# Optimization experiments

Hardware: AMD Instinct MI355X
Metric: run time of the kernel (lower is better)

Reference implementation:

```python
import jax, jax.numpy as jnp
import numpy as np
from jax import lax

B, T = 128, 512
V, D = 100000, 100   # word vocab, word embedding dim
H = 100              # per-direction LSTM hidden (concat -> 200)
L = 25               # number of CRF labels


def setup_inputs() -> dict:
    key = jax.random.key(0)
    ks = jax.random.split(key, 16)
    s = 0.02
    inp = {
        "tok_tensor": jax.random.randint(ks[0], (B, T), 0, V, dtype=jnp.int32),
        "tag_tensor": jax.random.randint(ks[1], (B, T), 0, L, dtype=jnp.int32),
        "lengths": jnp.full((B,), T, dtype=jnp.int32),
        "word_emb": jax.random.normal(ks[2], (V, D), jnp.float32) * s,
        # forward-direction LSTM (PyTorch gate order i,f,g,o)
        "w_ih_f": jax.random.normal(ks[3], (4 * H, D), jnp.float32) * s,
        "w_hh_f": jax.random.normal(ks[4], (4 * H, H), jnp.float32) * s,
        "b_ih_f": jax.random.normal(ks[5], (4 * H,), jnp.float32) * s,
        "b_hh_f": jax.random.normal(ks[6], (4 * H,), jnp.float32) * s,
        # backward-direction LSTM
        "w_ih_b": jax.random.normal(ks[7], (4 * H, D), jnp.float32) * s,
        "w_hh_b": jax.random.normal(ks[8], (4 * H, H), jnp.float32) * s,
        "b_ih_b": jax.random.normal(ks[9], (4 * H,), jnp.float32) * s,
        "b_hh_b": jax.random.normal(ks[10], (4 * H,), jnp.float32) * s,
        # hidden2tag linear
        "w_tag": jax.random.normal(ks[11], (L, 2 * H), jnp.float32) * s,
        "b_tag": jax.random.normal(ks[12], (L,), jnp.float32) * s,
        # CRF params
        "transitions": jax.random.normal(ks[13], (L, L), jnp.float32) * 0.1,
        "start_trans": jax.random.normal(ks[14], (L,), jnp.float32) * 0.1,
        "end_trans": jax.random.normal(ks[15], (L,), jnp.float32) * 0.1,
    }
    return inp


def _lstm(x_tbd, w_ih, w_hh, b_ih, b_hh, reverse):
    """x_tbd: [T,B,D] -> hidden states [T,B,H], aligned with input time axis."""
    Bh = x_tbd.shape[1]
    Hh = w_hh.shape[1]
    h0 = jnp.zeros((Bh, Hh), x_tbd.dtype)
    c0 = jnp.zeros((Bh, Hh), x_tbd.dtype)

    def step(carry, xt):
        h, c = carry
        gates = xt @ w_ih.T + b_ih + h @ w_hh.T + b_hh
        i, f, g, o = jnp.split(gates, 4, axis=-1)
        i = jax.nn.sigmoid(i); f = jax.nn.sigmoid(f)
        g = jnp.tanh(g); o = jax.nn.sigmoid(o)
        c = f * c + i * g
        h = o * jnp.tanh(c)
        return (h, c), h

    _, hs = lax.scan(step, (h0, c0), x_tbd, reverse=reverse)
    return hs


def _crf_nll(emissions, tags, mask, transitions, start_trans, end_trans):
    """Sum over batch of -(gold path score - log partition).
    emissions: [B,T,L], tags: [B,T] int, mask: [B,T] float (1=valid)."""
    Bb = emissions.shape[0]
    b_idx = jnp.arange(Bb)
    em_t = emissions.transpose(1, 0, 2)   # [T,B,L]
    tags_t = tags.T                       # [T,B]
    mask_t = mask.T                       # [T,B]

    # --- gold path score ---
    first_tags = tags_t[0]
    score0 = start_trans[first_tags] + em_t[0][b_idx, first_tags]

    def num_step(score, inp):
        em, tp, tc, m = inp  # emissions[t], tags[t-1], tags[t], mask[t]
        s = transitions[tp, tc] + em[b_idx, tc]
        return score + m * s, None

    gold, _ = lax.scan(num_step, score0,
                       (em_t[1:], tags_t[:-1], tags_t[1:], mask_t[1:]))
    last_idx = jnp.sum(mask, axis=1).astype(jnp.int32) - 1
    last_tags = tags[b_idx, last_idx]
    gold = gold + end_trans[last_tags]

    # --- log partition (forward algorithm) ---
    alpha0 = start_trans + em_t[0]  # [B,L]

    def part_step(alpha, inp):
        em, m = inp
        # [B,L_prev,1] + [L_prev,L_next] + [B,1,L_next]
        nxt = jax.nn.logsumexp(alpha[:, :, None] + transitions[None] + em[:, None, :], axis=1)
        alpha = jnp.where(m[:, None] > 0, nxt, alpha)
        return alpha, None

    alpha, _ = lax.scan(part_step, alpha0, (em_t[1:], mask_t[1:]))
    logZ = jax.nn.logsumexp(alpha + end_trans, axis=1)
    return jnp.sum(logZ - gold)


def reference(tok_tensor, tag_tensor, lengths,
              word_emb, w_ih_f, w_hh_f, b_ih_f, b_hh_f,
              w_ih_b, w_hh_b, b_ih_b, b_hh_b,
              w_tag, b_tag, transitions, start_trans, end_trans):
    # word embedding lookup: [B,T,D]
    tok_embs = word_emb[tok_tensor]
    x_tbd = tok_embs.transpose(1, 0, 2)  # [T,B,D]
    # BiLSTM encoder (dropout off: eval / deterministic reference)
    h_fwd = _lstm(x_tbd, w_ih_f, w_hh_f, b_ih_f, b_hh_f, reverse=False)
    h_bwd = _lstm(x_tbd, w_ih_b, w_hh_b, b_ih_b, b_hh_b, reverse=True)
    seq = jnp.concatenate([h_fwd, h_bwd], axis=-1).transpose(1, 0, 2)  # [B,T,2H]
    # hidden2tag
    emissions = jnp.einsum('btd,ld->btl', seq, w_tag) + b_tag  # [B,T,L]
    # CRF negative log-likelihood
    mask = (jnp.arange(T)[None, :] < lengths[:, None]).astype(emissions.dtype)
    return _crf_nll(emissions, tag_tensor, mask, transitions, start_trans, end_trans)
```

## Files before the change

### kernel.cpp

```cpp
#include <hip/hip_runtime.h>
#include <cstdint>
#include <cstddef>

#define BB 128
#define TT 512
#define DD 100
#define HH 100
#define NG 400
#define LL 25
#define TS 32
#define NTILE 16
#define F_LOG2E 1.44269504088896340736f
#define F_LN2   0.69314718055994530942f

typedef __decltype(__builtin_amdgcn_cvt_pkrtz(0.f, 0.f)) h2_t;
typedef _Float16 v8h __attribute__((ext_vector_type(8)));
typedef float v4f __attribute__((ext_vector_type(4)));

__device__ __forceinline__ h2_t bc_h2(unsigned int u) {
  return __builtin_bit_cast(h2_t, u);
}
__device__ __forceinline__ unsigned int pk(float x, float y) {
  return __builtin_bit_cast(unsigned int, __builtin_amdgcn_cvt_pkrtz(x, y));
}

__device__ __forceinline__ float fdot2(h2_t a, h2_t b, float c) {
#if __has_builtin(__builtin_amdgcn_fdot2)
  return __builtin_amdgcn_fdot2(a, b, c, false);
#else
  return c + (float)a[0] * (float)b[0] + (float)a[1] * (float)b[1];
#endif
}

__device__ __forceinline__ float fexp2(float x) { return __builtin_amdgcn_exp2f(x); }
__device__ __forceinline__ float flog2(float x) { return __builtin_amdgcn_logf(x); }
__device__ __forceinline__ float frcp(float x)  { return __builtin_amdgcn_rcpf(x); }

__device__ __forceinline__ float sigmoid_f(float x) {
  return frcp(1.f + fexp2(-F_LOG2E * x));
}
__device__ __forceinline__ float tanh_f(float x) {
  float e = fexp2(2.f * F_LOG2E * x);
  return 1.f - 2.f * frcp(e + 1.f);
}

template <int CTRL>
__device__ __forceinline__ float qadd(float v) {
#if __has_builtin(__builtin_amdgcn_mov_dpp)
  int m = __builtin_amdgcn_mov_dpp(__builtin_bit_cast(int, v), CTRL, 0xF, 0xF, true);
  return v + __builtin_bit_cast(float, m);
#else
  int x = (CTRL == 177) ? 1 : 2;
  return v + __shfl_xor(v, x);
#endif
}

template <int LANE>
__device__ __forceinline__ float qbcast(float v) {
#if __has_builtin(__builtin_amdgcn_mov_dpp)
  int m = __builtin_amdgcn_mov_dpp(__builtin_bit_cast(int, v), LANE * 0x55, 0xF, 0xF, true);
  return __builtin_bit_cast(float, m);
#else
  return __shfl(v, (threadIdx.x & 63 & ~3) + LANE);
#endif
}

__device__ __forceinline__ float bperm(float v, int byteidx) {
  return __builtin_bit_cast(float,
      __builtin_amdgcn_ds_bpermute(byteidx, __builtin_bit_cast(int, v)));
}
__device__ __forceinline__ float rfl(float v) {
  return __builtin_bit_cast(float,
      __builtin_amdgcn_readfirstlane(__builtin_bit_cast(int, v)));
}

__device__ __forceinline__ void lds_barrier() {
  __builtin_amdgcn_s_waitcnt(0xC07F);
  __builtin_amdgcn_s_barrier();
}

__global__ __launch_bounds__(512, 2) void lstm_fused2(
    const int* __restrict__ tok, const float* __restrict__ emb,
    const float* __restrict__ w_ih_f, const float* __restrict__ w_ih_b,
    const float* __restrict__ b_ih_f, const float* __restrict__ b_hh_f,
    const float* __restrict__ b_ih_b, const float* __restrict__ b_hh_b,
    const float* __restrict__ w_hh_f, const float* __restrict__ w_hh_b,
    const float* __restrict__ w_tag, const float* __restrict__ b_tag,
    float* __restrict__ em_f, float* __restrict__ em_b)
{
  const int tid = threadIdx.x;
  const int b   = blockIdx.x & 127;
  const int dir = blockIdx.x >> 7;
  const float* w_hh = dir ? w_hh_b : w_hh_f;
  const float* w_ih = dir ? w_ih_b : w_ih_f;
  const float* b_ih = dir ? b_ih_b : b_ih_f;
  const float* b_hh = dir ? b_hh_b : b_hh_f;

  __shared__ __align__(16) unsigned int wlds[400 * 68];
  __shared__ __align__(16) unsigned short gin_lds[TS * 400];
  __shared__ __align__(16) unsigned int xlds[TS * 68];
  __shared__ __align__(16) unsigned int hls0[52];
  __shared__ __align__(16) unsigned int hls1[52];

  for (int i = tid; i < 400 * 25; i += 512) {
    int row = i / 25;
    int q = i - row * 25;
    const float4 v = *(const float4*)(w_ih + (size_t)row * DD + 4 * q);
    wlds[row * 68 + 2 * q]     = pk(v.x, v.y);
    wlds[row * 68 + 2 * q + 1] = pk(v.z, v.w);
  }
  for (int i = tid; i < 400 * 18; i += 512) {
    int row = i / 18;
    int d = i - row * 18;
    wlds[row * 68 + 50 + d] = 0u;
  }
  for (int i = tid; i < TS * 18; i += 512) {
    int row = i / 18;
    int d = i - row * 18;
    xlds[row * 68 + 50 + d] = 0u;
  }

  const bool uact = tid < NG;
  const int j = tid >> 2;
  const int s = tid & 3;
  const int od = 12 * s;
  const int nnv = (s == 3) ? 14 : 12;

  h2_t wA[14], wB[14], wC[14], wD[14];
  float bias = 0.f;
  if (uact) {
#pragma unroll
    for (int d = 0; d < 14; ++d) {
      int dd = (d < nnv) ? (od + d) : 0;
      const float* r0 = w_hh + (size_t)(0 * 100 + j) * HH + 2 * dd;
      const float* r1 = w_hh + (size_t)(1 * 100 + j) * HH + 2 * dd;
      const float* r2 = w_hh + (size_t)(2 * 100 + j) * HH + 2 * dd;
      const float* r3 = w_hh + (size_t)(3 * 100 + j) * HH + 2 * dd;
      h2_t z = __builtin_amdgcn_cvt_pkrtz(0.f, 0.f);
      wA[d] = (d < nnv) ? __builtin_amdgcn_cvt_pkrtz(r0[0], r0[1]) : z;
      wB[d] = (d < nnv) ? __builtin_amdgcn_cvt_pkrtz(r1[0], r1[1]) : z;
      wC[d] = (d < nnv) ? __builtin_amdgcn_cvt_pkrtz(r2[0], r2[1]) : z;
      wD[d] = (d < nnv) ? __builtin_amdgcn_cvt_pkrtz(r3[0], r3[1]) : z;
    }
    bias = b_ih[s * 100 + j] + b_hh[s * 100 + j];
  }
  const float kk2 = (s == 2) ? (2.f * F_LOG2E) : (-F_LOG2E);
  const float cA  = (s == 2) ? -2.f : 1.f;
  const float cB  = (s == 2) ? 1.f : 0.f;

  const int el = tid - 448;
  const bool eact = (el >= 0) && (el < 50);
  const int l  = (el >= 0) ? (el >> 1) : 0;
  const int hf = (el >= 0) ? (el & 1) : 0;
  const int eo = hf ? 24 : 0;
  const int en = hf ? 26 : 24;
  h2_t wt[26];
  float bt = 0.f;
  if (eact) {
    const float* wr = w_tag + (size_t)l * 200 + dir * 100;
#pragma unroll
    for (int d = 0; d < 26; ++d) {
      int dd = (d < en) ? (eo + d) : 0;
      h2_t z = __builtin_amdgcn_cvt_pkrtz(0.f, 0.f);
      wt[d] = (d < en) ? __builtin_amdgcn_cvt_pkrtz(wr[2 * dd], wr[2 * dd + 1]) : z;
    }
    if (dir == 0 && hf == 0) bt = b_tag[l];
  }
  float* emo = dir ? em_b : em_f;
  float* emp = emo + ((size_t)b * TT + (dir ? (TT - 1) : 0)) * LL + l;
  const ptrdiff_t estep = dir ? -(ptrdiff_t)LL : (ptrdiff_t)LL;

  if (tid < 52) { hls0[tid] = 0u; hls1[tid] = 0u; }

  const int wv   = tid >> 6;
  const int lane = tid & 63;
  const int l16  = lane & 15;
  const int quad = lane >> 4;
  const int c0b  = (25 * wv) >> 3;
  const int c1b  = (25 * (wv + 1)) >> 3;

  const int tprow = tid / 13;
  const int tps   = tid - 13 * tprow;
  const bool tp_act = tid < 416;

  float4 xa = {0, 0, 0, 0}, xb = {0, 0, 0, 0};
  if (tp_act) {
    int ii = tprow;
    int tt = dir ? (TT - 1 - ii) : ii;
    int tk = tok[b * TT + tt];
    const float* xp = emb + (size_t)tk * DD + 8 * tps;
    xa = *(const float4*)xp;
    if (tps < 12) xb = *(const float4*)(xp + 4);
  }

  float c = 0.f;
  unsigned short gnext = 0;
  int grow = 0;

#define SDOT(d, hh) \
  p0 = fdot2(wA[d], bc_h2(hh), p0); p1 = fdot2(wB[d], bc_h2(hh), p1); \
  p2 = fdot2(wC[d], bc_h2(hh), p2); p3 = fdot2(wD[d], bc_h2(hh), p3);
#define EDOT(d, hh) { h2_t h = bc_h2(hh); \
  if ((d & 3) == 0) a0 = fdot2(wt[d], h, a0); \
  else if ((d & 3) == 1) a1 = fdot2(wt[d], h, a1); \
  else if ((d & 3) == 2) a2 = fdot2(wt[d], h, a2); \
  else a3 = fdot2(wt[d], h, a3); }

#define SCAN_STEP(HRD, HWR, TVNZ)                                          \
  {                                                                        \
    if (uact) {                                                            \
      unsigned short gcurr = gnext;                                        \
      int nr = (grow < TS - 1) ? grow + 1 : TS - 1;                        \
      gnext = gin_lds[nr * 400 + tid];                                     \
      grow = nr;                                                           \
      const unsigned int* hp = (HRD) + od;                                 \
      uint4 u0 = *((const uint4*)hp);                                      \
      uint4 u1 = *((const uint4*)(hp + 4));                                \
      uint4 u2 = *((const uint4*)(hp + 8));                                \
      uint2 u3 = *((const uint2*)(hp + 12));                               \
      float p0, p1, p2, p3;                                                \
      p0 = fdot2(wA[0], bc_h2(u0.x), 0.f);                                 \
      p1 = fdot2(wB[0], bc_h2(u0.x), 0.f);                                 \
      p2 = fdot2(wC[0], bc_h2(u0.x), 0.f);                                 \
      p3 = fdot2(wD[0], bc_h2(u0.x), 0.f);                                 \
      SDOT(1, u0.y)  SDOT(2, u0.z)  SDOT(3, u0.w)                          \
      SDOT(4, u1.x)  SDOT(5, u1.y)  SDOT(6, u1.z)  SDOT(7, u1.w)           \
      SDOT(8, u2.x)  SDOT(9, u2.y)  SDOT(10, u2.z) SDOT(11, u2.w)          \
      SDOT(12, u3.x) SDOT(13, u3.y)                                        \
      p0 = qadd<78>(qadd<177>(p0));                                        \
      p1 = qadd<78>(qadd<177>(p1));                                        \
      p2 = qadd<78>(qadd<177>(p2));                                        \
      p3 = qadd<78>(qadd<177>(p3));                                        \
      float psel = (s == 0) ? p0 : (s == 1) ? p1 : (s == 2) ? p2 : p3;     \
      float gate = psel + bias + (float)__builtin_bit_cast(__fp16, gcurr); \
      float y  = fexp2(kk2 * gate);                                        \
      float rr = frcp(1.f + y);                                            \
      float actv = fmaf(cA, rr, cB);                                       \
      float iv = qbcast<0>(actv);                                          \
      float fv = qbcast<1>(actv);                                          \
      float gv = qbcast<2>(actv);                                          \
      float ov = qbcast<3>(actv);                                          \
      c = fmaf(fv, c, iv * gv);                                            \
      float hvv = ov * tanh_f(c);                                          \
      if (s == 0) ((__fp16*)(HWR))[j] = (__fp16)hvv;                       \
    } else if (eact && (TVNZ)) {                                           \
      const unsigned int* hp = (HRD) + eo;                                 \
      uint4 e0 = *((const uint4*)hp);                                      \
      uint4 e1 = *((const uint4*)(hp + 4));                                \
      uint4 e2 = *((const uint4*)(hp + 8));                                \
      uint4 e3 = *((const uint4*)(hp + 12));                               \
      uint4 e4 = *((const uint4*)(hp + 16));                               \
      uint4 e5 = *((const uint4*)(hp + 20));                               \
      uint2 e6 = *((const uint2*)(hp + 24));                               \
      float a0, a1, a2, a3;                                                \
      a0 = fdot2(wt[0], bc_h2(e0.x), 0.f);                                 \
      a1 = fdot2(wt[1], bc_h2(e0.y), 0.f);                                 \
      a2 = fdot2(wt[2], bc_h2(e0.z), 0.f);                                 \
      a3 = fdot2(wt[3], bc_h2(e0.w), 0.f);                                 \
      EDOT(4, e1.x)  EDOT(5, e1.y)  EDOT(6, e1.z)  EDOT(7, e1.w)           \
      EDOT(8, e2.x)  EDOT(9, e2.y)  EDOT(10, e2.z) EDOT(11, e2.w)          \
      EDOT(12, e3.x) EDOT(13, e3.y) EDOT(14, e3.z) EDOT(15, e3.w)          \
      EDOT(16, e4.x) EDOT(17, e4.y) EDOT(18, e4.z) EDOT(19, e4.w)          \
      EDOT(20, e5.x) EDOT(21, e5.y) EDOT(22, e5.z) EDOT(23, e5.w)          \
      EDOT(24, e6.x) EDOT(25, e6.y)                                        \
      float ss = (a0 + a1) + (a2 + a3);                                    \
      float tot = qadd<177>(ss);                                           \
      if (hf == 0) *emp = tot + bt;                                        \
      emp += estep;                                                        \
    }                                                                      \
    lds_barrier();                                                         \
  }

  __syncthreads();

  for (int T = 0; T < NTILE; ++T) {
    if (tp_act) {
      unsigned int* xr = xlds + tprow * 68 + 4 * tps;
      if (tps < 12) {
        uint4 u;
        u.x = pk(xa.x, xa.y); u.y = pk(xa.z, xa.w);
        u.z = pk(xb.x, xb.y); u.w = pk(xb.z, xb.w);
        *(uint4*)xr = u;
      } else {
        xr[0] = pk(xa.x, xa.y);
        xr[1] = pk(xa.z, xa.w);
      }
    }
    __syncthreads();

    {
      v8h af[2][4];
#pragma unroll
      for (int rg = 0; rg < 2; ++rg)
#pragma unroll
        for (int f = 0; f < 4; ++f)
          af[rg][f] = __builtin_bit_cast(v8h,
              *(const uint4*)(xlds + (rg * 16 + l16) * 68 + f * 16 + quad * 4));

      if (tp_act && T + 1 < NTILE) {
        int ii = (T + 1) * TS + tprow;
        int tt = dir ? (TT - 1 - ii) : ii;
        int tk = tok[b * TT + tt];
        const float* xp = emb + (size_t)tk * DD + 8 * tps;
        xa = *(const float4*)xp;
        if (tps < 12) xb = *(const float4*)(xp + 4);
      }

      __fp16* gout = (__fp16*)gin_lds;
      for (int cc = c0b; cc < c1b; ++cc) {
        const int n = 16 * cc + l16;
        const unsigned int* wp = wlds + n * 68 + quad * 4;
        v8h bf0 = __builtin_bit_cast(v8h, *(const uint4*)(wp));
        v8h bf1 = __builtin_bit_cast(v8h, *(const uint4*)(wp + 16));
        v8h bf2 = __builtin_bit_cast(v8h, *(const uint4*)(wp + 32));
        v8h bf3 = __builtin_bit_cast(v8h, *(const uint4*)(wp + 48));
        const int qn = (n * 41) >> 12;
        const int p  = ((n - 100 * qn) << 2) + qn;
#pragma unroll
        for (int rg = 0; rg < 2; ++rg) {
          v4f acc = {0.f, 0.f, 0.f, 0.f};
          acc = __builtin_amdgcn_mfma_f32_16x16x32_f16(af[rg][0], bf0, acc, 0, 0, 0);
          acc = __builtin_amdgcn_mfma_f32_16x16x32_f16(af[rg][1], bf1, acc, 0, 0, 0);
          acc = __builtin_amdgcn_mfma_f32_16x16x32_f16(af[rg][2], bf2, acc, 0, 0, 0);
          acc = __builtin_amdgcn_mfma_f32_16x16x32_f16(af[rg][3], bf3, acc, 0, 0, 0);
          const int rowb = rg * 16 + quad * 4;
#pragma unroll
          for (int r = 0; r < 4; ++r)
            gout[(rowb + r) * 400 + p] = (__fp16)acc[r];
        }
      }
    }
    __syncthreads();
    if (uact) { grow = 0; gnext = gin_lds[tid]; }

    SCAN_STEP(hls0, hls1, (T > 0))
    SCAN_STEP(hls1, hls0, true)
    for (int it = 1; it < TS / 2; ++it) {
      SCAN_STEP(hls0, hls1, true)
      SCAN_STEP(hls1, hls0, true)
    }
  }
#undef SCAN_STEP
#undef SDOT

  if (eact) {
    const unsigned int* hp = hls0 + eo;
    uint4 e0 = *((const uint4*)hp);
    uint4 e1 = *((const uint4*)(hp + 4));
    uint4 e2 = *((const uint4*)(hp + 8));
    uint4 e3 = *((const uint4*)(hp + 12));
    uint4 e4 = *((const uint4*)(hp + 16));
    uint4 e5 = *((const uint4*)(hp + 20));
    uint2 e6 = *((const uint2*)(hp + 24));
    float a0, a1, a2, a3;
    a0 = fdot2(wt[0], bc_h2(e0.x), 0.f);
    a1 = fdot2(wt[1], bc_h2(e0.y), 0.f);
    a2 = fdot2(wt[2], bc_h2(e0.z), 0.f);
    a3 = fdot2(wt[3], bc_h2(e0.w), 0.f);
    EDOT(4, e1.x)  EDOT(5, e1.y)  EDOT(6, e1.z)  EDOT(7, e1.w)
    EDOT(8, e2.x)  EDOT(9, e2.y)  EDOT(10, e2.z) EDOT(11, e2.w)
    EDOT(12, e3.x) EDOT(13, e3.y) EDOT(14, e3.z) EDOT(15, e3.w)
    EDOT(16, e4.x) EDOT(17, e4.y) EDOT(18, e4.z) EDOT(19, e4.w)
    EDOT(20, e5.x) EDOT(21, e5.y) EDOT(22, e5.z) EDOT(23, e5.w)
    EDOT(24, e6.x) EDOT(25, e6.y)
    float ss = (a0 + a1) + (a2 + a3);
    float tot = qadd<177>(ss);
    if (hf == 0) {
      int ttp = dir ? 0 : (TT - 1);
      emo[((size_t)b * TT + ttp) * LL + l] = tot + bt;
    }
  }
#undef EDOT
}

__global__ __launch_bounds__(512, 2) void lstm_scan_fb(
    const int* __restrict__ tok, const float* __restrict__ emb,
    const float* __restrict__ w_ih_f, const float* __restrict__ w_hh_f,
    const float* __restrict__ b_ih_f, const float* __restrict__ b_hh_f,
    const float* __restrict__ w_ih_b, const float* __restrict__ w_hh_b,
    const float* __restrict__ b_ih_b, const float* __restrict__ b_hh_b,
    unsigned short* __restrict__ hc16)
{
  const int tid = threadIdx.x;
  const int b   = blockIdx.x & 127;
  const int dir = blockIdx.x >> 7;

  const float* w_ih = dir ? w_ih_b : w_ih_f;
  const float* w_hh = dir ? w_hh_b : w_hh_f;
  const float* b_ih = dir ? b_ih_b : b_ih_f;
  const float* b_hh = dir ? b_hh_b : b_hh_f;

  __shared__ __align__(16) unsigned int xs[2][64];
  __shared__ __align__(16) unsigned int hls[64];
  __shared__ float gl[NG];

  h2_t wih[50], whh[50];
  float bias = 0.f;
  if (tid < NG) {
    const float4* wi = (const float4*)(w_ih + tid * DD);
    const float4* wh = (const float4*)(w_hh + tid * DD);
#pragma unroll
    for (int kk = 0; kk < 25; ++kk) {
      float4 a = wi[kk];
      wih[2 * kk]     = __builtin_amdgcn_cvt_pkrtz(a.x, a.y);
      wih[2 * kk + 1] = __builtin_amdgcn_cvt_pkrtz(a.z, a.w);
      float4 c = wh[kk];
      whh[2 * kk]     = __builtin_amdgcn_cvt_pkrtz(c.x, c.y);
      whh[2 * kk + 1] = __builtin_amdgcn_cvt_pkrtz(c.z, c.w);
    }
    bias = b_ih[tid] + b_hh[tid];
  }
  if (tid < 2) { xs[0][50 + tid] = 0u; xs[1][50 + tid] = 0u; hls[50 + tid] = 0u; }
  if (tid < 50) hls[tid] = 0u;

  const int base = b * TT;
  if (tid >= 448 && tid < 498) {
    int tt0 = dir ? (TT - 1) : 0;
    int i = tid - 448;
    int tk = tok[base + tt0];
    float2 v = ((const float2*)(emb + (size_t)tk * DD))[i];
    xs[0][i] = pk(v.x, v.y);
  }
  __syncthreads();

  float cst = 0.f;
  unsigned short* hcb = hc16 + (size_t)base * 200 + dir * 100;

  for (int t = 0; t < TT; ++t) {
    const int buf = t & 1;
    const int tt  = dir ? (TT - 1 - t) : t;

    if (tid < NG) {
      float a0 = bias, a1 = 0.f, a2 = 0.f, a3 = 0.f;
      const unsigned int* xp = xs[buf];
#pragma unroll
      for (int g = 0; g < 13; ++g) {
        uint4 u = ((const uint4*)xp)[g];
        const int k = 4 * g;
        a0 = fdot2(wih[k], bc_h2(u.x), a0);
        a1 = fdot2(wih[k + 1], bc_h2(u.y), a1);
        if (k + 2 < 50) a2 = fdot2(wih[k + 2], bc_h2(u.z), a2);
        if (k + 3 < 50) a3 = fdot2(wih[k + 3], bc_h2(u.w), a3);
      }
#pragma unroll
      for (int g = 0; g < 13; ++g) {
        uint4 u = ((const uint4*)hls)[g];
        const int k = 4 * g;
        a0 = fdot2(whh[k], bc_h2(u.x), a0);
        a1 = fdot2(whh[k + 1], bc_h2(u.y), a1);
        if (k + 2 < 50) a2 = fdot2(whh[k + 2], bc_h2(u.z), a2);
        if (k + 3 < 50) a3 = fdot2(whh[k + 3], bc_h2(u.w), a3);
      }
      float accs = (a0 + a1) + (a2 + a3);
      float av = (tid >= 200 && tid < 300) ? tanh_f(accs) : sigmoid_f(accs);
      gl[tid] = av;
    } else if (tid >= 448 && tid < 498 && t < TT - 1) {
      int ttn = dir ? (TT - 2 - t) : (t + 1);
      int i = tid - 448;
      int tk = tok[base + ttn];
      float2 v = ((const float2*)(emb + (size_t)tk * DD))[i];
      xs[buf ^ 1][i] = pk(v.x, v.y);
    }
    __syncthreads();

    if (tid < HH) {
      float gi = gl[tid], gf = gl[tid + 100], gg = gl[tid + 200], go = gl[tid + 300];
      cst = gf * cst + gi * gg;
      float hv = go * tanh_f(cst);
      __fp16 h16 = (__fp16)hv;
      ((__fp16*)hls)[tid] = h16;
      hcb[(size_t)tt * 200 + tid] = __builtin_bit_cast(unsigned short, h16);
    }
    __syncthreads();
  }
}

__global__ __launch_bounds__(256, 2) void emis2(
    const unsigned short* __restrict__ hc16, const float* __restrict__ w_tag,
    const float* __restrict__ b_tag, float* __restrict__ em)
{
  __shared__ unsigned int hsh[64 * 101];
  __shared__ unsigned int wsh[25 * 100];
  const int tid = threadIdx.x;
  const size_t m0 = (size_t)blockIdx.x * 64;

  const unsigned int* hcu = (const unsigned int*)hc16;
  for (int i = tid; i < 64 * 100; i += 256) {
    int r = i / 100;
    int k = i - r * 100;
    hsh[r * 101 + k] = hcu[m0 * 100 + i];
  }
  for (int i = tid; i < 25 * 100; i += 256) {
    float2 wv = ((const float2*)w_tag)[i];
    wsh[i] = pk(wv.x, wv.y);
  }
  __syncthreads();

  const int r = tid & 63, q = tid >> 6;
  int lidx[7];
  bool lv[7];
  float acc[7];
#pragma unroll
  for (int ii = 0; ii < 7; ++ii) {
    int l = q + 4 * ii;
    lv[ii] = (l < LL);
    lidx[ii] = lv[ii] ? l : 0;
    acc[ii] = lv[ii] ? b_tag[lidx[ii]] : 0.f;
  }
  const unsigned int* hrow = hsh + r * 101;
#pragma unroll 2
  for (int k = 0; k < 100; ++k) {
    h2_t hv = bc_h2(hrow[k]);
#pragma unroll
    for (int ii = 0; ii < 7; ++ii)
      acc[ii] = fdot2(hv, bc_h2(wsh[lidx[ii] * 100 + k]), acc[ii]);
  }
#pragma unroll
  for (int ii = 0; ii < 7; ++ii)
    if (lv[ii]) em[(m0 + r) * LL + lidx[ii]] = acc[ii];
}

__global__ __launch_bounds__(192) void crf_all(
    const float* __restrict__ em_f, const float* __restrict__ em_b,
    const int* __restrict__ tags, const int* __restrict__ lengths,
    const float* __restrict__ trans,
    const float* __restrict__ startt, const float* __restrict__ endt,
    float* __restrict__ out)
{
  const int tid = threadIdx.x;
  const int b   = blockIdx.x;
  const int w   = tid >> 6;
  const int lane = tid & 63;

  __shared__ float abf[LL], abb[LL];
  __shared__ float gd;

  if (w < 2) {
    const int side = w;
    const int j = (lane < LL) ? lane : 0;
    const float* ef = em_f + (size_t)b * TT * LL;
    const float* eb = em_b + (size_t)b * TT * LL;

    float E[LL];
#pragma unroll
    for (int i = 0; i < LL; ++i) {
      float tv = (side == 0 ? trans[i * LL + j] : trans[j * LL + i]);
      E[i] = fexp2(tv * F_LOG2E);
    }

    float a, C = 0.f;
    if (side == 0) {
      a = (startt[j] + ef[j] + eb[j]) * F_LOG2E;
      float efA = ef[LL + j],     ebA = eb[LL + j];
      float efB = ef[2 * LL + j], ebB = eb[2 * LL + j];
      for (int t = 1; t < 256; ++t) {
        float em2 = (efA + ebA) * F_LOG2E;
        int tn = (t + 2 < 256) ? (t + 2) : 255;
        efA = efB; ebA = ebB;
        efB = ef[(size_t)tn * LL + j];
        ebB = eb[(size_t)tn * LL + j];
        float sh = rfl(a);
        C += sh;
        float A = fexp2(a - sh);
        float s0 = 0.f, s1 = 0.f, s2 = 0.f, s3 = 0.f;
#pragma unroll
        for (int i = 0; i < LL; ++i) {
          float Ai = bperm(A, 4 * i);
          if ((i & 3) == 0) s0 = fmaf(Ai, E[i], s0);
          else if ((i & 3) == 1) s1 = fmaf(Ai, E[i], s1);
          else if ((i & 3) == 2) s2 = fmaf(Ai, E[i], s2);
          else s3 = fmaf(Ai, E[i], s3);
        }
        a = flog2((s0 + s1) + (s2 + s3)) + em2;
      }
    } else {
      a = endt[j] * F_LOG2E;
      float efA = ef[(size_t)(TT - 1) * LL + j], ebA = eb[(size_t)(TT - 1) * LL + j];
      float efB = ef[(size_t)(TT - 2) * LL + j], ebB = eb[(size_t)(TT - 2) * LL + j];
      for (int stpi = 0; stpi < 256; ++stpi) {
        float em2 = (efA + ebA) * F_LOG2E;
        int t1n = (stpi + 2 < 256) ? (TT - 3 - stpi) : 256;
        efA = efB; ebA = ebB;
        efB = ef[(size_t)t1n * LL + j];
        ebB = eb[(size_t)t1n * LL + j];
        float v = a + em2;
        float sh = rfl(v);
        C += sh;
        float A = fexp2(v - sh);
        float s0 = 0.f, s1 = 0.f, s2 = 0.f, s3 = 0.f;
#pragma unroll
        for (int i = 0; i < LL; ++i) {
          float Ai = bperm(A, 4 * i);
          if ((i & 3) == 0) s0 = fmaf(Ai, E[i], s0);
          else if ((i & 3) == 1) s1 = fmaf(Ai, E[i], s1);
          else if ((i & 3) == 2) s2 = fmaf(Ai, E[i], s2);
          else s3 = fmaf(Ai, E[i], s3);
        }
        a = flog2((s0 + s1) + (s2 + s3));
      }
    }
    if (lane < LL) {
      if (side == 0) abf[lane] = a + C;
      else          abb[lane] = a + C;
    }
  } else {
    const int len = lengths[b];
    float acc = 0.f;
#pragma unroll
    for (int k = 0; k < 8; ++k) {
      int t = k * 64 + lane;
      int tg = tags[b * TT + t];
      size_t ei = ((size_t)b * TT + t) * LL + tg;
      float e = em_f[ei] + em_b[ei];
      float term;
      if (t == 0) term = startt[tg] + e;
      else        term = trans[tags[b * TT + t - 1] * LL + tg] + e;
      if (t == len - 1) term += endt[tg];
      if (t < len) acc += term;
    }
    for (int o = 32; o > 0; o >>= 1) acc += __shfl_down(acc, o);
    if (lane == 0) gd = acc;
  }
  __syncthreads();

  if (tid < 64) {
    float v = (tid < LL) ? (abf[tid] + abb[tid]) : -1e30f;
    float m = v;
    for (int o = 32; o > 0; o >>= 1) m = fmaxf(m, __shfl_down(m, o));
    m = rfl(m);
    float e = (tid < LL) ? fexp2(v - m) : 0.f;
    for (int o = 32; o > 0; o >>= 1) e += __shfl_down(e, o);
    if (tid == 0)
      atomicAdd(out, (m + flog2(e)) * F_LN2 - gd);
  }
}

extern "C" void kernel_launch(void* const* d_in, const int* in_sizes, int n_in,
                              void* d_out, int out_size, void* d_ws, size_t ws_size,
                              hipStream_t stream) {
  const int*   tok   = (const int*)d_in[0];
  const int*   tags  = (const int*)d_in[1];
  const int*   lens  = (const int*)d_in[2];
  const float* emb   = (const float*)d_in[3];
  const float* wif   = (const float*)d_in[4];
  const float* whf   = (const float*)d_in[5];
  const float* bif   = (const float*)d_in[6];
  const float* bhf   = (const float*)d_in[7];
  const float* wib   = (const float*)d_in[8];
  const float* whb   = (const float*)d_in[9];
  const float* bib   = (const float*)d_in[10];
  const float* bhb   = (const float*)d_in[11];
  const float* wtag  = (const float*)d_in[12];
  const float* btag  = (const float*)d_in[13];
  const float* trans = (const float*)d_in[14];
  const float* st    = (const float*)d_in[15];
  const float* en    = (const float*)d_in[16];

  char* wsb = (char*)d_ws;
  float* em_f = (float*)wsb;
  float* em_b = (float*)(wsb + 6553600);
  const size_t need_fused = 13107200ULL;
  const size_t need_fb    = 13107200ULL + 26214400ULL;

  hipMemsetAsync(d_out, 0, sizeof(float), stream);

  if (ws_size >= need_fused && ws_size < need_fb) {
    lstm_fused2<<<256, 512, 0, stream>>>(tok, emb, wif, wib, bif, bhf, bib, bhb,
                                         whf, whb, wtag, btag, em_f, em_b);
  } else if (ws_size >= need_fb) {
    lstm_fused2<<<256, 512, 0, stream>>>(tok, emb, wif, wib, bif, bhf, bib, bhb,
                                         whf, whb, wtag, btag, em_f, em_b);
  } else {
    unsigned short* hc16 = (unsigned short*)(wsb + 13107200);
    hipMemsetAsync(em_b, 0, 6553600, stream);
    lstm_scan_fb<<<256, 512, 0, stream>>>(tok, emb, wif, whf, bif, bhf,
                                          wib, whb, bib, bhb, hc16);
    emis2<<<1024, 256, 0, stream>>>(hc16, wtag, btag, em_f);
  }
  crf_all<<<128, 192, 0, stream>>>(em_f, em_b, tags, lens, trans, st, en,
                                   (float*)d_out);
}
```

Baseline: 433.1 us.

## Keep input-projection weights in MFMA registers and use LDS broadcast in CRF scan

New measurement: 424.9 us (median of 2 runs). No clear change (-1.9%).

```diff
diff --git a/kernel.cpp b/kernel.cpp
--- a/kernel.cpp
+++ b/kernel.cpp
@@ -65,21 +65,23 @@
 #endif
 }
 
-__device__ __forceinline__ float bperm(float v, int byteidx) {
-  return __builtin_bit_cast(float,
-      __builtin_amdgcn_ds_bpermute(byteidx, __builtin_bit_cast(int, v)));
-}
 __device__ __forceinline__ float rfl(float v) {
   return __builtin_bit_cast(float,
       __builtin_amdgcn_readfirstlane(__builtin_bit_cast(int, v)));
 }
 
+__device__ __forceinline__ void wave_fence() {
+#if __has_builtin(__builtin_amdgcn_wave_barrier)
+  __builtin_amdgcn_wave_barrier();
+#endif
+}
+
 __device__ __forceinline__ void lds_barrier() {
   __builtin_amdgcn_s_waitcnt(0xC07F);
   __builtin_amdgcn_s_barrier();
 }
 
-__global__ __launch_bounds__(512, 2) void lstm_fused2(
+__global__ __launch_bounds__(512, 2) void lstm_fused3(
     const int* __restrict__ tok, const float* __restrict__ emb,
     const float* __restrict__ w_ih_f, const float* __restrict__ w_ih_b,
     const float* __restrict__ b_ih_f, const float* __restrict__ b_hh_f,
@@ -96,24 +98,48 @@
   const float* b_ih = dir ? b_ih_b : b_ih_f;
   const float* b_hh = dir ? b_hh_b : b_hh_f;
 
-  __shared__ __align__(16) unsigned int wlds[400 * 68];
   __shared__ __align__(16) unsigned short gin_lds[TS * 400];
   __shared__ __align__(16) unsigned int xlds[TS * 68];
   __shared__ __align__(16) unsigned int hls0[52];
   __shared__ __align__(16) unsigned int hls1[52];
 
-  for (int i = tid; i < 400 * 25; i += 512) {
-    int row = i / 25;
-    int q = i - row * 25;
-    const float4 v = *(const float4*)(w_ih + (size_t)row * DD + 4 * q);
-    wlds[row * 68 + 2 * q]     = pk(v.x, v.y);
-    wlds[row * 68 + 2 * q + 1] = pk(v.z, v.w);
-  }
-  for (int i = tid; i < 400 * 18; i += 512) {
-    int row = i / 18;
-    int d = i - row * 18;
-    wlds[row * 68 + 50 + d] = 0u;
-  }
+  const int wv   = tid >> 6;
+  const int lane = tid & 63;
+  const int l16  = lane & 15;
+  const int quad = lane >> 4;
+  const int c0b  = (25 * wv) >> 3;
+  const int c1b  = (25 * (wv + 1)) >> 3;
+  const int ncol = c1b - c0b;
+
+  v8h bfr[4][4];
+  int pcol[4];
+#pragma unroll
+  for (int ci = 0; ci < 4; ++ci) {
+    const int cc = (ci < ncol) ? (c0b + ci) : c0b;
+    const int n  = 16 * cc + l16;
+    const float* wr = w_ih + (size_t)n * DD;
+#pragma unroll
+    for (int f = 0; f < 3; ++f) {
+      const float* wp = wr + f * 32 + quad * 8;
+      float4 va = *(const float4*)(wp);
+      float4 vb = *(const float4*)(wp + 4);
+      uint4 u;
+      u.x = pk(va.x, va.y); u.y = pk(va.z, va.w);
+      u.z = pk(vb.x, vb.y); u.w = pk(vb.z, vb.w);
+      bfr[ci][f] = __builtin_bit_cast(v8h, u);
+    }
+    {
+      uint4 u = {0u, 0u, 0u, 0u};
+      if (quad == 0) {
+        float4 va = *(const float4*)(wr + 96);
+        u.x = pk(va.x, va.y); u.y = pk(va.z, va.w);
+      }
+      bfr[ci][3] = __builtin_bit_cast(v8h, u);
+    }
+    const int qn = (n * 41) >> 12;
+    pcol[ci] = ((n - 100 * qn) << 2) + qn;
+  }
+
   for (int i = tid; i < TS * 18; i += 512) {
     int row = i / 18;
     int d = i - row * 18;
@@ -171,13 +197,6 @@
   const ptrdiff_t estep = dir ? -(ptrdiff_t)LL : (ptrdiff_t)LL;
 
   if (tid < 52) { hls0[tid] = 0u; hls1[tid] = 0u; }
-
-  const int wv   = tid >> 6;
-  const int lane = tid & 63;
-  const int l16  = lane & 15;
-  const int quad = lane >> 4;
-  const int c0b  = (25 * wv) >> 3;
-  const int c1b  = (25 * (wv + 1)) >> 3;
 
   const int tprow = tid / 13;
   const int tps   = tid - 13 * tprow;
@@ -307,22 +326,17 @@
       }
 
       __fp16* gout = (__fp16*)gin_lds;
-      for (int cc = c0b; cc < c1b; ++cc) {
-        const int n = 16 * cc + l16;
-        const unsigned int* wp = wlds + n * 68 + quad * 4;
-        v8h bf0 = __builtin_bit_cast(v8h, *(const uint4*)(wp));
-        v8h bf1 = __builtin_bit_cast(v8h, *(const uint4*)(wp + 16));
-        v8h bf2 = __builtin_bit_cast(v8h, *(const uint4*)(wp + 32));
-        v8h bf3 = __builtin_bit_cast(v8h, *(const uint4*)(wp + 48));
-        const int qn = (n * 41) >> 12;
-        const int p  = ((n - 100 * qn) << 2) + qn;
+#pragma unroll
+      for (int ci = 0; ci < 4; ++ci) {
+        if (ci >= ncol) break;
+        const int p = pcol[ci];
 #pragma unroll
         for (int rg = 0; rg < 2; ++rg) {
           v4f acc = {0.f, 0.f, 0.f, 0.f};
-          acc = __builtin_amdgcn_mfma_f32_16x16x32_f16(af[rg][0], bf0, acc, 0, 0, 0);
-          acc = __builtin_amdgcn_mfma_f32_16x16x32_f16(af[rg][1], bf1, acc, 0, 0, 0);
-          acc = __builtin_amdgcn_mfma_f32_16x16x32_f16(af[rg][2], bf2, acc, 0, 0, 0);
-          acc = __builtin_amdgcn_mfma_f32_16x16x32_f16(af[rg][3], bf3, acc, 0, 0, 0);
+          acc = __builtin_amdgcn_mfma_f32_16x16x32_f16(af[rg][0], bfr[ci][0], acc, 0, 0, 0);
+          acc = __builtin_amdgcn_mfma_f32_16x16x32_f16(af[rg][1], bfr[ci][1], acc, 0, 0, 0);
+          acc = __builtin_amdgcn_mfma_f32_16x16x32_f16(af[rg][2], bfr[ci][2], acc, 0, 0, 0);
+          acc = __builtin_amdgcn_mfma_f32_16x16x32_f16(af[rg][3], bfr[ci][3], acc, 0, 0, 0);
           const int rowb = rg * 16 + quad * 4;
 #pragma unroll
           for (int r = 0; r < 4; ++r)
@@ -373,154 +387,7 @@
 #undef EDOT
 }
 
-__global__ __launch_bounds__(512, 2) void lstm_scan_fb(
-    const int* __restrict__ tok, const float* __restrict__ emb,
-    const float* __restrict__ w_ih_f, const float* __restrict__ w_hh_f,
-    const float* __restrict__ b_ih_f, const float* __restrict__ b_hh_f,
-    const float* __restrict__ w_ih_b, const float* __restrict__ w_hh_b,
-    const float* __restrict__ b_ih_b, const float* __restrict__ b_hh_b,
-    unsigned short* __restrict__ hc16)
-{
-  const int tid = threadIdx.x;
-  const int b   = blockIdx.x & 127;
-  const int dir = blockIdx.x >> 7;
-
-  const float* w_ih = dir ? w_ih_b : w_ih_f;
-  const float* w_hh = dir ? w_hh_b : w_hh_f;
-  const float* b_ih = dir ? b_ih_b : b_ih_f;
-  const float* b_hh = dir ? b_hh_b : b_hh_f;
-
-  __shared__ __align__(16) unsigned int xs[2][64];
-  __shared__ __align__(16) unsigned int hls[64];
-  __shared__ float gl[NG];
-
-  h2_t wih[50], whh[50];
-  float bias = 0.f;
-  if (tid < NG) {
-    const float4* wi = (const float4*)(w_ih + tid * DD);
-    const float4* wh = (const float4*)(w_hh + tid * DD);
-#pragma unroll
-    for (int kk = 0; kk < 25; ++kk) {
-      float4 a = wi[kk];
-      wih[2 * kk]     = __builtin_amdgcn_cvt_pkrtz(a.x, a.y);
-      wih[2 * kk + 1] = __builtin_amdgcn_cvt_pkrtz(a.z, a.w);
-      float4 c = wh[kk];
-      whh[2 * kk]     = __builtin_amdgcn_cvt_pkrtz(c.x, c.y);
-      whh[2 * kk + 1] = __builtin_amdgcn_cvt_pkrtz(c.z, c.w);
-    }
-    bias = b_ih[tid] + b_hh[tid];
-  }
-  if (tid < 2) { xs[0][50 + tid] = 0u; xs[1][50 + tid] = 0u; hls[50 + tid] = 0u; }
-  if (tid < 50) hls[tid] = 0u;
-
-  const int base = b * TT;
-  if (tid >= 448 && tid < 498) {
-    int tt0 = dir ? (TT - 1) : 0;
-    int i = tid - 448;
-    int tk = tok[base + tt0];
-    float2 v = ((const float2*)(emb + (size_t)tk * DD))[i];
-    xs[0][i] = pk(v.x, v.y);
-  }
-  __syncthreads();
-
-  float cst = 0.f;
-  unsigned short* hcb = hc16 + (size_t)base * 200 + dir * 100;
-
-  for (int t = 0; t < TT; ++t) {
-    const int buf = t & 1;
-    const int tt  = dir ? (TT - 1 - t) : t;
-
-    if (tid < NG) {
-      float a0 = bias, a1 = 0.f, a2 = 0.f, a3 = 0.f;
-      const unsigned int* xp = xs[buf];
-#pragma unroll
-      for (int g = 0; g < 13; ++g) {
-        uint4 u = ((const uint4*)xp)[g];
-        const int k = 4 * g;
-        a0 = fdot2(wih[k], bc_h2(u.x), a0);
-        a1 = fdot2(wih[k + 1], bc_h2(u.y), a1);
-        if (k + 2 < 50) a2 = fdot2(wih[k + 2], bc_h2(u.z), a2);
-        if (k + 3 < 50) a3 = fdot2(wih[k + 3], bc_h2(u.w), a3);
-      }
-#pragma unroll
-      for (int g = 0; g < 13; ++g) {
-        uint4 u = ((const uint4*)hls)[g];
-        const int k = 4 * g;
-        a0 = fdot2(whh[k], bc_h2(u.x), a0);
-        a1 = fdot2(whh[k + 1], bc_h2(u.y), a1);
-        if (k + 2 < 50) a2 = fdot2(whh[k + 2], bc_h2(u.z), a2);
-        if (k + 3 < 50) a3 = fdot2(whh[k + 3], bc_h2(u.w), a3);
-      }
-      float accs = (a0 + a1) + (a2 + a3);
-      float av = (tid >= 200 && tid < 300) ? tanh_f(accs) : sigmoid_f(accs);
-      gl[tid] = av;
-    } else if (tid >= 448 && tid < 498 && t < TT - 1) {
-      int ttn = dir ? (TT - 2 - t) : (t + 1);
-      int i = tid - 448;
-      int tk = tok[base + ttn];
-      float2 v = ((const float2*)(emb + (size_t)tk * DD))[i];
-      xs[buf ^ 1][i] = pk(v.x, v.y);
-    }
-    __syncthreads();
-
-    if (tid < HH) {
-      float gi = gl[tid], gf = gl[tid + 100], gg = gl[tid + 200], go = gl[tid + 300];
-      cst = gf * cst + gi * gg;
-      float hv = go * tanh_f(cst);
-      __fp16 h16 = (__fp16)hv;
-      ((__fp16*)hls)[tid] = h16;
-      hcb[(size_t)tt * 200 + tid] = __builtin_bit_cast(unsigned short, h16);
-    }
-    __syncthreads();
-  }
-}
-
-__global__ __launch_bounds__(256, 2) void emis2(
-    const unsigned short* __restrict__ hc16, const float* __restrict__ w_tag,
-    const float* __restrict__ b_tag, float* __restrict__ em)
-{
-  __shared__ unsigned int hsh[64 * 101];
-  __shared__ unsigned int wsh[25 * 100];
-  const int tid = threadIdx.x;
-  const size_t m0 = (size_t)blockIdx.x * 64;
-
-  const unsigned int* hcu = (const unsigned int*)hc16;
-  for (int i = tid; i < 64 * 100; i += 256) {
-    int r = i / 100;
-    int k = i - r * 100;
-    hsh[r * 101 + k] = hcu[m0 * 100 + i];
-  }
-  for (int i = tid; i < 25 * 100; i += 256) {
-    float2 wv = ((const float2*)w_tag)[i];
-    wsh[i] = pk(wv.x, wv.y);
-  }
-  __syncthreads();
-
-  const int r = tid & 63, q = tid >> 6;
-  int lidx[7];
-  bool lv[7];
-  float acc[7];
-#pragma unroll
-  for (int ii = 0; ii < 7; ++ii) {
-    int l = q + 4 * ii;
-    lv[ii] = (l < LL);
-    lidx[ii] = lv[ii] ? l : 0;
-    acc[ii] = lv[ii] ? b_tag[lidx[ii]] : 0.f;
-  }
-  const unsigned int* hrow = hsh + r * 101;
-#pragma unroll 2
-  for (int k = 0; k < 100; ++k) {
-    h2_t hv = bc_h2(hrow[k]);
-#pragma unroll
-    for (int ii = 0; ii < 7; ++ii)
-      acc[ii] = fdot2(hv, bc_h2(wsh[lidx[ii] * 100 + k]), acc[ii]);
-  }
-#pragma unroll
-  for (int ii = 0; ii < 7; ++ii)
-    if (lv[ii]) em[(m0 + r) * LL + lidx[ii]] = acc[ii];
-}
-
-__global__ __launch_bounds__(192) void crf_all(
+__global__ __launch_bounds__(192) void crf_all2(
     const float* __restrict__ em_f, const float* __restrict__ em_b,
     const int* __restrict__ tags, const int* __restrict__ lengths,
     const float* __restrict__ trans,
@@ -532,20 +399,53 @@
   const int w   = tid >> 6;
   const int lane = tid & 63;
 
+  __shared__ __align__(16) float As[2][32];
   __shared__ float abf[LL], abb[LL];
   __shared__ float gd;
+
+  if (w < 2 && lane >= LL && lane < 32) As[w][lane] = 0.f;
 
   if (w < 2) {
     const int side = w;
     const int j = (lane < LL) ? lane : 0;
     const float* ef = em_f + (size_t)b * TT * LL;
     const float* eb = em_b + (size_t)b * TT * LL;
-
-    float E[LL];
+    float* Aw = As[side];
+    const float4* Ap = (const float4*)Aw;
+
+    float E[28];
 #pragma unroll
     for (int i = 0; i < LL; ++i) {
       float tv = (side == 0 ? trans[i * LL + j] : trans[j * LL + i]);
       E[i] = fexp2(tv * F_LOG2E);
+    }
+    E[25] = 0.f; E[26] = 0.f; E[27] = 0.f;
+
+#define LSE_STEP(vin, aout)                                                \
+    {                                                                      \
+      float sh = rfl(vin);                                                 \
+      C += sh;                                                             \
+      float A = fexp2((vin) - sh);                                         \
+      if (lane < LL) Aw[lane] = A;                                         \
+      wave_fence();                                                        \
+      float4 q0 = Ap[0], q1 = Ap[1], q2 = Ap[2], q3 = Ap[3];               \
+      float4 q4 = Ap[4], q5 = Ap[5], q6 = Ap[6];                           \
+      float s0, s1, s2, s3;                                                \
+      s0 = q0.x * E[0];  s1 = q0.y * E[1];                                 \
+      s2 = q0.z * E[2];  s3 = q0.w * E[3];                                 \
+      s0 = fmaf(q1.x, E[4], s0);  s1 = fmaf(q1.y, E[5], s1);               \
+      s2 = fmaf(q1.z, E[6], s2);  s3 = fmaf(q1.w, E[7], s3);               \
+      s0 = fmaf(q2.x, E[8], s0);  s1 = fmaf(q2.y, E[9], s1);               \
+      s2 = fmaf(q2.z, E[10], s2); s3 = fmaf(q2.w, E[11], s3);              \
+      s0 = fmaf(q3.x, E[12], s0); s1 = fmaf(q3.y, E[13], s1);              \
+      s2 = fmaf(q3.z, E[14], s2); s3 = fmaf(q3.w, E[15], s3);              \
+      s0 = fmaf(q4.x, E[16], s0); s1 = fmaf(q4.y, E[17], s1);              \
+      s2 = fmaf(q4.z, E[18], s2); s3 = fmaf(q4.w, E[19], s3);              \
+      s0 = fmaf(q5.x, E[20], s0); s1 = fmaf(q5.y, E[21], s1);              \
+      s2 = fmaf(q5.z, E[22], s2); s3 = fmaf(q5.w, E[23], s3);              \
+      s0 = fmaf(q6.x, E[24], s0); s1 = fmaf(q6.y, E[25], s1);              \
+      s2 = fmaf(q6.z, E[26], s2); s3 = fmaf(q6.w, E[27], s3);              \
+      aout = flog2((s0 + s1) + (s2 + s3));                                 \
     }
 
     float a, C = 0.f;
@@ -559,19 +459,9 @@
         efA = efB; ebA = ebB;
         efB = ef[(size_t)tn * LL + j];
         ebB = eb[(size_t)tn * LL + j];
-        float sh = rfl(a);
-        C += sh;
-        float A = fexp2(a - sh);
-        float s0 = 0.f, s1 = 0.f, s2 = 0.f, s3 = 0.f;
-#pragma unroll
-        for (int i = 0; i < LL; ++i) {
-          float Ai = bperm(A, 4 * i);
-          if ((i & 3) == 0) s0 = fmaf(Ai, E[i], s0);
-          else if ((i & 3) == 1) s1 = fmaf(Ai, E[i], s1);
-          else if ((i & 3) == 2) s2 = fmaf(Ai, E[i], s2);
-          else s3 = fmaf(Ai, E[i], s3);
-        }
-        a = flog2((s0 + s1) + (s2 + s3)) + em2;
+        float nx;
+        LSE_STEP(a, nx)
+        a = nx + em2;
       }
     } else {
       a = endt[j] * F_LOG2E;
@@ -584,21 +474,10 @@
         efB = ef[(size_t)t1n * LL + j];
         ebB = eb[(size_t)t1n * LL + j];
         float v = a + em2;
-        float sh = rfl(v);
-        C += sh;
-        float A = fexp2(v - sh);
-        float s0 = 0.f, s1 = 0.f, s2 = 0.f, s3 = 0.f;
-#pragma unroll
-        for (int i = 0; i < LL; ++i) {
-          float Ai = bperm(A, 4 * i);
-          if ((i & 3) == 0) s0 = fmaf(Ai, E[i], s0);
-          else if ((i & 3) == 1) s1 = fmaf(Ai, E[i], s1);
-          else if ((i & 3) == 2) s2 = fmaf(Ai, E[i], s2);
-          else s3 = fmaf(Ai, E[i], s3);
-        }
-        a = flog2((s0 + s1) + (s2 + s3));
+        LSE_STEP(v, a)
       }
     }
+#undef LSE_STEP
     if (lane < LL) {
       if (side == 0) abf[lane] = a + C;
       else          abb[lane] = a + C;
@@ -659,24 +538,11 @@
   char* wsb = (char*)d_ws;
   float* em_f = (float*)wsb;
   float* em_b = (float*)(wsb + 6553600);
-  const size_t need_fused = 13107200ULL;
-  const size_t need_fb    = 13107200ULL + 26214400ULL;
 
   hipMemsetAsync(d_out, 0, sizeof(float), stream);
 
-  if (ws_size >= need_fused && ws_size < need_fb) {
-    lstm_fused2<<<256, 512, 0, stream>>>(tok, emb, wif, wib, bif, bhf, bib, bhb,
-                                         whf, whb, wtag, btag, em_f, em_b);
-  } else if (ws_size >= need_fb) {
-    lstm_fused2<<<256, 512, 0, stream>>>(tok, emb, wif, wib, bif, bhf, bib, bhb,
-                                         whf, whb, wtag, btag, em_f, em_b);
-  } else {
-    unsigned short* hc16 = (unsigned short*)(wsb + 13107200);
-    hipMemsetAsync(em_b, 0, 6553600, stream);
-    lstm_scan_fb<<<256, 512, 0, stream>>>(tok, emb, wif, whf, bif, bhf,
-                                          wib, whb, bib, bhb, hc16);
-    emis2<<<1024, 256, 0, stream>>>(hc16, wtag, btag, em_f);
-  }
-  crf_all<<<128, 192, 0, stream>>>(em_f, em_b, tags, lens, trans, st, en,
-                                   (float*)d_out);
-}
+  lstm_fused3<<<256, 512, 0, stream>>>(tok, emb, wif, wib, bif, bhf, bib, bhb,
+                                       whf, whb, wtag, btag, em_f, em_b);
+  crf_all2<<<128, 192, 0, stream>>>(em_f, em_b, tags, lens, trans, st, en,
+                                    (float*)d_out);
+}
```
